# Kernel tuning notes

Measured on AMD Instinct MI355X. Metric: run time of the kernel, lower is better.

The kernel has to match this reference:

```python
import jax, jax.numpy as jnp
import numpy as np

N, E, D, H = 50000, 500000, 160, 5
C = D // H          # per-head channels = 32
MLP_H = 50          # hidden_dim of output MLP
NEG_SLOPE = 0.2
EPS = 1e-5


def layer_norm(x, g, b):
    mu = jnp.mean(x, axis=-1, keepdims=True)
    var = jnp.mean((x - mu) ** 2, axis=-1, keepdims=True)
    return (x - mu) / jnp.sqrt(var + EPS) * g + b


def setup_inputs() -> dict:
    key = jax.random.key(0)
    ks = jax.random.split(key, 24)
    s_d = 1.0 / np.sqrt(D)
    s_h = 1.0 / np.sqrt(MLP_H)
    inp = {
        "x": jax.random.normal(ks[0], (N, D), jnp.float32),
        "edge_index": jax.random.randint(ks[1], (2, E), 0, N, jnp.int32),
        "edge_attr": jax.random.normal(ks[2], (E, D), jnp.float32),
        "u": jax.random.normal(ks[3], (1, 16), jnp.float32),
        "batch": jnp.zeros((N,), jnp.int32),
        # GATv2Conv params (lin_l, lin_r, lin_edge, att, out bias)
        "Wl": jax.random.normal(ks[4], (D, H * C), jnp.float32) * s_d,
        "bl": jnp.zeros((H * C,), jnp.float32),
        "Wr": jax.random.normal(ks[5], (D, H * C), jnp.float32) * s_d,
        "br": jnp.zeros((H * C,), jnp.float32),
        "We": jax.random.normal(ks[6], (D, H * C), jnp.float32) * s_d,
        "att": jax.random.normal(ks[7], (H, C), jnp.float32) * (1.0 / np.sqrt(C)),
        "bias": jnp.zeros((H * C,), jnp.float32),
        # norm1
        "g1": jnp.ones((D,), jnp.float32),
        "beta1": jnp.zeros((D,), jnp.float32),
        # output MLP: Linear(D,50) -> SELU -> LN(50) -> Linear(50,D)
        "W1": jax.random.normal(ks[8], (D, MLP_H), jnp.float32) * s_d,
        "b1": jnp.zeros((MLP_H,), jnp.float32),
        "gm": jnp.ones((MLP_H,), jnp.float32),
        "bm": jnp.zeros((MLP_H,), jnp.float32),
        "W2": jax.random.normal(ks[9], (MLP_H, D), jnp.float32) * s_h,
        "b2": jnp.zeros((D,), jnp.float32),
        # norm2
        "g2": jnp.ones((D,), jnp.float32),
        "beta2": jnp.zeros((D,), jnp.float32),
    }
    return inp


def gatv2(x, edge_index, edge_attr, Wl, bl, Wr, br, We, att, bias):
    src, dst = edge_index[0], edge_index[1]
    xl = (x @ Wl + bl).reshape(N, H, C)   # source transform (x_j)
    xr = (x @ Wr + br).reshape(N, H, C)   # target transform (x_i)
    ea = (edge_attr @ We).reshape(E, H, C)
    m = xl[src] + xr[dst] + ea            # [E,H,C]
    score = jnp.einsum('ehc,hc->eh', jax.nn.leaky_relu(m, NEG_SLOPE), att)  # [E,H]
    # softmax over incoming edges of each destination node
    smax = jax.ops.segment_max(score, dst, num_segments=N)  # [N,H]
    sexp = jnp.exp(score - smax[dst])
    ssum = jax.ops.segment_sum(sexp, dst, num_segments=N)   # [N,H]
    alpha = sexp / jnp.where(ssum == 0.0, 1.0, ssum)[dst]   # [E,H]
    out = jax.ops.segment_sum(xl[src] * alpha[:, :, None], dst, num_segments=N)
    return out.reshape(N, H * C) + bias


def reference(x, edge_index, edge_attr, u, batch,
              Wl, bl, Wr, br, We, att, bias,
              g1, beta1, W1, b1, gm, bm, W2, b2, g2, beta2):
    attn = gatv2(x, edge_index, edge_attr, Wl, bl, Wr, br, We, att, bias)
    h = layer_norm(x + attn, g1, beta1)
    mlp = layer_norm(jax.nn.selu(h @ W1 + b1), gm, bm) @ W2 + b2
    return layer_norm(h + mlp, g2, beta2)
```

## Files before the change

kernel.cpp:

```cpp
#include <hip/hip_runtime.h>

#define NNODES 50000
#define NEDGES 500000
#define DIM    160
#define NHEAD  5
#define MLPH   50

typedef __bf16 bf16x8 __attribute__((ext_vector_type(8)));
typedef float  f32x4  __attribute__((ext_vector_type(4)));

#define PB_WLT   0
#define PB_WRT   25600
#define PB_WET   51200
#define PB_W1    76800
#define PB_W2    84800
#define PB_VEC   92800
#define PB_SMALL 94240
#define PB_TOTAL 94400

struct Ptrs {
    const void *Wl, *Wr, *We;
    const void *bl, *br, *att, *bias, *g1, *beta1;
    const void *W1, *b1, *gm, *bm, *W2, *b2, *g2, *beta2;
};

__device__ __forceinline__ float ldany(const void* p, long i, bool f32) {
    return f32 ? ((const float*)p)[i] : (float)(((const __bf16*)p)[i]);
}

__global__ void detect_kernel(const unsigned short* __restrict__ xs, int* __restrict__ flag) {
    __shared__ int red[4];
    int cnt = 0;
    for (int i = threadIdx.x; i < 65536; i += 256) {
        unsigned e = (xs[i] >> 7) & 0xFFu;
        if (e >= 137u) cnt++;
    }
    for (int off = 1; off < 64; off <<= 1) cnt += __shfl_xor(cnt, off, 64);
    if ((threadIdx.x & 63) == 0) red[threadIdx.x >> 6] = cnt;
    __syncthreads();
    if (threadIdx.x == 0) flag[0] = (red[0] + red[1] + red[2] + red[3] > 1000) ? 1 : 0;
}

__global__ void prep_kernel(Ptrs p, __bf16* __restrict__ pb, const int* __restrict__ flag) {
    const bool f32 = flag[0] != 0;
    int i = blockIdx.x * 256 + threadIdx.x;
    if (i < 76800) {
        int which = i / 25600, r = i - which * 25600;
        int n = r / DIM, k = r - n * DIM;
        const void* w = which == 0 ? p.Wl : which == 1 ? p.Wr : p.We;
        pb[i] = (__bf16)ldany(w, (long)k * DIM + n, f32);
    } else if (i < 84800) {
        pb[i] = (__bf16)ldany(p.W1, i - PB_W1, f32);
    } else if (i < 92800) {
        pb[i] = (__bf16)ldany(p.W2, i - PB_W2, f32);
    } else if (i < 94240) {
        int t = i - PB_VEC, which = t / DIM, off = t - which * DIM;
        const void* v = which == 0 ? p.bl : which == 1 ? p.br : which == 2 ? p.att :
                        which == 3 ? p.bias : which == 4 ? p.g1 : which == 5 ? p.beta1 :
                        which == 6 ? p.b2 : which == 7 ? p.g2 : p.beta2;
        pb[i] = (__bf16)ldany(v, off, f32);
    } else if (i < 94390) {
        int t = i - PB_SMALL;
        const void* v = t < 50 ? p.b1 : t < 100 ? p.gm : p.bm;
        pb[i] = (__bf16)ldany(v, t % 50, f32);
    }
}

template <bool DO_SCORE>
__global__ __launch_bounds__(256, 2) void gemm160(
    const void* __restrict__ A, long M,
    const __bf16* __restrict__ Bt,
    const __bf16* __restrict__ bias,
    __bf16* __restrict__ Cout,
    const __bf16* __restrict__ xl, const __bf16* __restrict__ xr,
    const int* __restrict__ src, const int* __restrict__ dst,
    const __bf16* __restrict__ att, float* __restrict__ score,
    int* __restrict__ cursor, int* __restrict__ psrc,
    const int* __restrict__ flag)
{
    __shared__ __bf16 Bts[DIM * DIM];
    __shared__ __bf16 As[128 * 32];
    const bool aF32 = flag[0] != 0;
    const int tid  = threadIdx.x;
    const int wave = tid >> 6, lane = tid & 63;
    const int quad = lane >> 4, l16 = lane & 15;
    const long blockRow = (long)blockIdx.x * 128;

    {
        const uint4* g = (const uint4*)Bt;
        uint4* s = (uint4*)Bts;
        for (int i = tid; i < DIM * DIM / 8; i += 256) s[i] = g[i];
    }

    const f32x4 zero4 = {0.f, 0.f, 0.f, 0.f};
    f32x4 acc[2][10];
#pragma unroll
    for (int r = 0; r < 2; r++)
#pragma unroll
        for (int n = 0; n < 10; n++) acc[r][n] = zero4;

    for (int k0 = 0; k0 < DIM; k0 += 32) {
        __syncthreads();
        for (int c = tid; c < 512; c += 256) {
            int row = c >> 2, col = (c & 3) * 8;
            long gr = blockRow + row;
            if (!aF32) {
                uint4 v = {0u, 0u, 0u, 0u};
                if (gr < M) v = *(const uint4*)((const __bf16*)A + gr * DIM + k0 + col);
                ((uint4*)As)[c] = v;
            } else {
                bf16x8 t = {};
                if (gr < M) {
                    const float* ap = (const float*)A + gr * DIM + k0 + col;
                    float4 f0 = *(const float4*)ap;
                    float4 f1 = *(const float4*)(ap + 4);
                    t[0] = (__bf16)f0.x; t[1] = (__bf16)f0.y;
                    t[2] = (__bf16)f0.z; t[3] = (__bf16)f0.w;
                    t[4] = (__bf16)f1.x; t[5] = (__bf16)f1.y;
                    t[6] = (__bf16)f1.z; t[7] = (__bf16)f1.w;
                }
                *(bf16x8*)(((uint4*)As) + c) = t;
            }
        }
        __syncthreads();
        bf16x8 a0 = *(const bf16x8*)(As + (wave * 32 + l16) * 32 + quad * 8);
        bf16x8 a1 = *(const bf16x8*)(As + (wave * 32 + 16 + l16) * 32 + quad * 8);
#pragma unroll
        for (int n = 0; n < 10; n++) {
            bf16x8 b = *(const bf16x8*)(Bts + (n * 16 + l16) * DIM + k0 + quad * 8);
            acc[0][n] = __builtin_amdgcn_mfma_f32_16x16x32_bf16(a0, b, acc[0][n], 0, 0, 0);
            acc[1][n] = __builtin_amdgcn_mfma_f32_16x16x32_bf16(a1, b, acc[1][n], 0, 0, 0);
        }
    }

    if (!DO_SCORE) {
#pragma unroll
        for (int r = 0; r < 2; r++)
#pragma unroll
            for (int n = 0; n < 10; n++) {
                int col = n * 16 + l16;
                float bv = (float)bias[col];
#pragma unroll
                for (int reg = 0; reg < 4; reg++) {
                    long row = blockRow + wave * 32 + r * 16 + quad * 4 + reg;
                    if (row < M) Cout[row * DIM + col] = (__bf16)(acc[r][n][reg] + bv);
                }
            }
    } else {
#pragma unroll
        for (int r = 0; r < 2; r++) {
            long erow[4]; int sv[4], dv[4]; int slot[4] = {0, 0, 0, 0};
#pragma unroll
            for (int reg = 0; reg < 4; reg++) {
                erow[reg] = blockRow + wave * 32 + r * 16 + quad * 4 + reg;
                long e = erow[reg] < M ? erow[reg] : M - 1;
                sv[reg] = src[e]; dv[reg] = dst[e];
            }
            if (l16 == 0) {
#pragma unroll
                for (int reg = 0; reg < 4; reg++)
                    if (erow[reg] < M) slot[reg] = atomicAdd(&cursor[dv[reg]], 1);
            }
#pragma unroll
            for (int hh = 0; hh < NHEAD; hh++) {
                float sacc[4] = {0.f, 0.f, 0.f, 0.f};
#pragma unroll
                for (int sub = 0; sub < 2; sub++) {
                    int n = hh * 2 + sub;
                    int col = n * 16 + l16;
                    float av = (float)att[col];
#pragma unroll
                    for (int reg = 0; reg < 4; reg++) {
                        float m = acc[r][n][reg]
                                + (float)xl[(long)sv[reg] * DIM + col]
                                + (float)xr[(long)dv[reg] * DIM + col];
                        m = m > 0.f ? m : 0.2f * m;
                        sacc[reg] += m * av;
                    }
                }
#pragma unroll
                for (int off = 1; off < 16; off <<= 1)
#pragma unroll
                    for (int reg = 0; reg < 4; reg++)
                        sacc[reg] += __shfl_xor(sacc[reg], off, 64);
                if (l16 == 0) {
#pragma unroll
                    for (int reg = 0; reg < 4; reg++)
                        if (erow[reg] < M) score[(long)slot[reg] * NHEAD + hh] = sacc[reg];
                }
            }
            if (l16 == 0) {
#pragma unroll
                for (int reg = 0; reg < 4; reg++)
                    if (erow[reg] < M) psrc[slot[reg]] = sv[reg];
            }
        }
    }
}

__global__ void hist_kernel(const int* __restrict__ dst, int* __restrict__ deg) {
    int e = blockIdx.x * 256 + threadIdx.x;
    if (e < NEDGES) atomicAdd(&deg[dst[e]], 1);
}

__global__ __launch_bounds__(256) void scan_kernel(const int* __restrict__ deg,
                                                   int* __restrict__ offs,
                                                   int* __restrict__ cursor) {
    __shared__ int part[256];
    const int t = threadIdx.x;
    const int chunk = (NNODES + 255) / 256;
    int beg = t * chunk;
    int end = beg + chunk; if (end > NNODES) end = NNODES;
    int s = 0;
    for (int i = beg; i < end; i++) s += deg[i];
    part[t] = s;
    __syncthreads();
    for (int off = 1; off < 256; off <<= 1) {
        int v = 0;
        if (t >= off) v = part[t - off];
        __syncthreads();
        part[t] += v;
        __syncthreads();
    }
    int run = (t == 0) ? 0 : part[t - 1];
    for (int i = beg; i < end; i++) {
        offs[i] = run; cursor[i] = run;
        run += deg[i];
    }
    if (t == 255) offs[NNODES] = run;
}

__global__ __launch_bounds__(256) void node_kernel(
    const int* __restrict__ offs, const int* __restrict__ psrc,
    const float* __restrict__ score,
    const __bf16* __restrict__ xl, const void* __restrict__ x,
    const __bf16* __restrict__ pb, const int* __restrict__ flag,
    __bf16* __restrict__ hout)
{
    const bool f32 = flag[0] != 0;
    const __bf16* bias  = pb + PB_VEC + 3 * DIM;
    const __bf16* g1    = pb + PB_VEC + 4 * DIM;
    const __bf16* beta1 = pb + PB_VEC + 5 * DIM;
    const int lane = threadIdx.x & 63;
    const long n = (long)blockIdx.x * 4 + (threadIdx.x >> 6);
    const int beg = offs[n], end = offs[n + 1];
    const int deg = end - beg;

    float mx[NHEAD];
#pragma unroll
    for (int h = 0; h < NHEAD; h++) mx[h] = -1e30f;
    for (int j = lane; j < deg; j += 64) {
        const float* sp = score + (long)(beg + j) * NHEAD;
#pragma unroll
        for (int h = 0; h < NHEAD; h++) mx[h] = fmaxf(mx[h], sp[h]);
    }
#pragma unroll
    for (int h = 0; h < NHEAD; h++)
#pragma unroll
        for (int off = 1; off < 64; off <<= 1)
            mx[h] = fmaxf(mx[h], __shfl_xor(mx[h], off, 64));

    float sm[NHEAD] = {0.f, 0.f, 0.f, 0.f, 0.f};
    float accv[3] = {0.f, 0.f, 0.f};
    for (int j0 = 0; j0 < deg; j0 += 64) {
        const int cn = min(deg - j0, 64);
        float w[NHEAD]; int si = 0;
        if (lane < cn) {
            const float* sp = score + (long)(beg + j0 + lane) * NHEAD;
#pragma unroll
            for (int h = 0; h < NHEAD; h++) {
                w[h] = expf(sp[h] - mx[h]);
                sm[h] += w[h];
            }
            si = psrc[beg + j0 + lane];
        } else {
#pragma unroll
            for (int h = 0; h < NHEAD; h++) w[h] = 0.f;
        }
        for (int j = 0; j < cn; j++) {
            const int sj = __shfl(si, j, 64);
            const float w0 = __shfl(w[0], j, 64);
            const float w1 = __shfl(w[1], j, 64);
            const float w2 = __shfl(w[2], j, 64);
            const float w3 = __shfl(w[3], j, 64);
            const float w4 = __shfl(w[4], j, 64);
            const __bf16* xrow = xl + (long)sj * DIM;
            accv[0] += (lane < 32 ? w0 : w1) * (float)xrow[lane];
            accv[1] += (lane < 32 ? w2 : w3) * (float)xrow[lane + 64];
            if (lane < 32) accv[2] += w4 * (float)xrow[lane + 128];
        }
    }
#pragma unroll
    for (int h = 0; h < NHEAD; h++)
#pragma unroll
        for (int off = 1; off < 64; off <<= 1)
            sm[h] += __shfl_xor(sm[h], off, 64);
    float ism[NHEAD];
#pragma unroll
    for (int h = 0; h < NHEAD; h++) ism[h] = sm[h] > 0.f ? 1.f / sm[h] : 0.f;
    accv[0] *= lane < 32 ? ism[0] : ism[1];
    accv[1] *= lane < 32 ? ism[2] : ism[3];
    accv[2] *= ism[4];

    const int nch = (lane < 32) ? 3 : 2;
    float v[3]; float s1 = 0.f, s2 = 0.f;
    for (int c = 0; c < nch; c++) {
        int ch = lane + c * 64;
        float xv = f32 ? ((const float*)x)[n * DIM + ch]
                       : (float)(((const __bf16*)x)[n * DIM + ch]);
        float t = accv[c] + (float)bias[ch] + xv;
        v[c] = t; s1 += t; s2 += t * t;
    }
    for (int off = 1; off < 64; off <<= 1) {
        s1 += __shfl_xor(s1, off, 64);
        s2 += __shfl_xor(s2, off, 64);
    }
    float mu = s1 * (1.f / DIM);
    float var = fmaxf(s2 * (1.f / DIM) - mu * mu, 0.f);
    float rs = rsqrtf(var + 1e-5f);
    for (int c = 0; c < nch; c++) {
        int ch = lane + c * 64;
        hout[n * DIM + ch] = (__bf16)((v[c] - mu) * rs * (float)g1[ch] + (float)beta1[ch]);
    }
}

__global__ __launch_bounds__(256, 2) void mlp_kernel(
    const __bf16* __restrict__ hmat, const __bf16* __restrict__ pb,
    float* __restrict__ out)
{
    __shared__ __bf16 W1s[DIM * MLPH];
    __shared__ __bf16 W2s[MLPH * DIM];
    __shared__ float hrow[4][DIM];
    __shared__ float zrow[4][MLPH];
    const __bf16* W1 = pb + PB_W1;
    const __bf16* W2 = pb + PB_W2;
    const __bf16* b2 = pb + PB_VEC + 6 * DIM;
    const __bf16* g2 = pb + PB_VEC + 7 * DIM;
    const __bf16* beta2 = pb + PB_VEC + 8 * DIM;
    const __bf16* b1 = pb + PB_SMALL;
    const __bf16* gm = pb + PB_SMALL + 50;
    const __bf16* bm = pb + PB_SMALL + 100;
    const int tid = threadIdx.x, wave = tid >> 6, lane = tid & 63;
    for (int i = tid; i < DIM * MLPH / 8; i += 256) {
        ((uint4*)W1s)[i] = ((const uint4*)W1)[i];
        ((uint4*)W2s)[i] = ((const uint4*)W2)[i];
    }
    __syncthreads();
    const int nch = (lane < 32) ? 3 : 2;
    for (int it = 0; it < 4; it++) {
        long n = (long)blockIdx.x * 16 + it * 4 + wave;
        float hv[3];
        for (int c = 0; c < nch; c++) {
            int ch = lane + c * 64;
            float t = (float)hmat[n * DIM + ch];
            hv[c] = t; hrow[wave][ch] = t;
        }
        __syncthreads();
        float z = 0.f;
        if (lane < MLPH) {
            z = (float)b1[lane];
            for (int k = 0; k < DIM; k++) z += hrow[wave][k] * (float)W1s[k * MLPH + lane];
            const float SC = 1.0507009873554805f, AL = 1.6732632423543772f;
            z = (z > 0.f) ? SC * z : SC * AL * (expf(z) - 1.f);
        }
        float s1 = (lane < MLPH) ? z : 0.f, s2 = (lane < MLPH) ? z * z : 0.f;
        for (int off = 1; off < 64; off <<= 1) {
            s1 += __shfl_xor(s1, off, 64);
            s2 += __shfl_xor(s2, off, 64);
        }
        float mu = s1 * (1.f / MLPH);
        float var = fmaxf(s2 * (1.f / MLPH) - mu * mu, 0.f);
        float rs = rsqrtf(var + 1e-5f);
        if (lane < MLPH) zrow[wave][lane] = (z - mu) * rs * (float)gm[lane] + (float)bm[lane];
        __syncthreads();
        float y[3], t1 = 0.f, t2 = 0.f;
        for (int c = 0; c < nch; c++) {
            int ch = lane + c * 64;
            float o = (float)b2[ch];
            for (int j = 0; j < MLPH; j++) o += zrow[wave][j] * (float)W2s[j * DIM + ch];
            float yy = hv[c] + o;
            y[c] = yy; t1 += yy; t2 += yy * yy;
        }
        for (int off = 1; off < 64; off <<= 1) {
            t1 += __shfl_xor(t1, off, 64);
            t2 += __shfl_xor(t2, off, 64);
        }
        float mu2 = t1 * (1.f / DIM);
        float var2 = fmaxf(t2 * (1.f / DIM) - mu2 * mu2, 0.f);
        float rs2 = rsqrtf(var2 + 1e-5f);
        for (int c = 0; c < nch; c++) {
            int ch = lane + c * 64;
            out[n * DIM + ch] = (y[c] - mu2) * rs2 * (float)g2[ch] + (float)beta2[ch];
        }
        __syncthreads();
    }
}

extern "C" void kernel_launch(void* const* d_in, const int* in_sizes, int n_in,
                              void* d_out, int out_size, void* d_ws, size_t ws_size,
                              hipStream_t stream)
{
    const void* x   = d_in[0];
    const int*  ei  = (const int*)d_in[1];
    const void* ea  = d_in[2];
    Ptrs p;
    p.Wl = d_in[5];  p.bl = d_in[6];  p.Wr = d_in[7];  p.br = d_in[8];
    p.We = d_in[9];  p.att = d_in[10]; p.bias = d_in[11];
    p.g1 = d_in[12]; p.beta1 = d_in[13];
    p.W1 = d_in[14]; p.b1 = d_in[15]; p.gm = d_in[16]; p.bm = d_in[17];
    p.W2 = d_in[18]; p.b2 = d_in[19]; p.g2 = d_in[20]; p.beta2 = d_in[21];
    const int* srcp = ei;
    const int* dstp = ei + NEDGES;

    char* ws = (char*)d_ws;
    int*    flag   = (int*)ws;    ws += 16;
    __bf16* pb     = (__bf16*)ws; ws += (size_t)PB_TOTAL * 2;
    int*    deg    = (int*)ws;    ws += (size_t)NNODES * 4;
    int*    offs   = (int*)ws;    ws += (size_t)(NNODES + 1) * 4 + 12;
    int*    cursor = (int*)ws;    ws += (size_t)NNODES * 4;
    int*    psrc   = (int*)ws;    ws += (size_t)NEDGES * 4;
    float*  score  = (float*)ws;  ws += (size_t)NEDGES * NHEAD * 4;
    __bf16* xl     = (__bf16*)ws; ws += (size_t)NNODES * DIM * 2;
    __bf16* xr     = (__bf16*)ws; ws += (size_t)NNODES * DIM * 2;
    __bf16* hbuf   = xr;
    const size_t NEEDED = (size_t)(ws - (char*)d_ws);

    if (ws_size < NEEDED) {
        return;
    }

    (void)hipMemsetAsync(deg, 0, (size_t)NNODES * 4, stream);

    detect_kernel<<<1, 256, 0, stream>>>((const unsigned short*)x, flag);
    prep_kernel<<<369, 256, 0, stream>>>(p, pb, flag);

    const int gemmN = (NNODES + 127) / 128;
    const int gemmE = (NEDGES + 127) / 128;
    gemm160<false><<<gemmN, 256, 0, stream>>>(x, NNODES, pb + PB_WLT, pb + PB_VEC + 0 * DIM, xl,
                                              nullptr, nullptr, nullptr, nullptr, nullptr, nullptr,
                                              nullptr, nullptr, flag);
    gemm160<false><<<gemmN, 256, 0, stream>>>(x, NNODES, pb + PB_WRT, pb + PB_VEC + 1 * DIM, xr,
                                              nullptr, nullptr, nullptr, nullptr, nullptr, nullptr,
                                              nullptr, nullptr, flag);

    hist_kernel<<<(NEDGES + 255) / 256, 256, 0, stream>>>(dstp, deg);
    scan_kernel<<<1, 256, 0, stream>>>(deg, offs, cursor);

    gemm160<true><<<gemmE, 256, 0, stream>>>(ea, NEDGES, pb + PB_WET, nullptr, nullptr,
                                             xl, xr, srcp, dstp, pb + PB_VEC + 2 * DIM, score,
                                             cursor, psrc, flag);

    node_kernel<<<NNODES / 4, 256, 0, stream>>>(offs, psrc, score, xl, x, pb, flag, hbuf);

    mlp_kernel<<<NNODES / 16, 256, 0, stream>>>(hbuf, pb, (float*)d_out);
}
```

Before: 1.086 ms.

## Load GEMM A operands directly into registers with prefetch, pad B smem, widen scan

The gemm160 kernel no longer stages A tiles through shared memory. Each lane loads its own A fragments straight from global memory into registers: the fp32 path double-buffers the next K chunk, and the bf16 path preloads all K chunks before the B copy. This removes per-K-step __syncthreads. The B tile is stored with a padded row stride of 168 to avoid LDS bank conflicts, and launch bounds are raised to 3 blocks per CU. The single-block scan is also widened from 256 to 1024 threads to shorten each thread's serial chunk. The trade-off is higher register pressure from the held fragments, which may spill under the new occupancy target.

```diff
diff --git a/kernel.cpp b/kernel.cpp
--- a/kernel.cpp
+++ b/kernel.cpp
@@ -67,7 +67,7 @@
 }
 
 template <bool DO_SCORE>
-__global__ __launch_bounds__(256, 2) void gemm160(
+__global__ __launch_bounds__(256, 3) void gemm160(
     const void* __restrict__ A, long M,
     const __bf16* __restrict__ Bt,
     const __bf16* __restrict__ bias,
@@ -78,19 +78,18 @@
     int* __restrict__ cursor, int* __restrict__ psrc,
     const int* __restrict__ flag)
 {
-    __shared__ __bf16 Bts[DIM * DIM];
-    __shared__ __bf16 As[128 * 32];
+    constexpr int BROW = 168;
+    __shared__ __bf16 Bts[DIM * BROW];
     const bool aF32 = flag[0] != 0;
     const int tid  = threadIdx.x;
     const int wave = tid >> 6, lane = tid & 63;
     const int quad = lane >> 4, l16 = lane & 15;
     const long blockRow = (long)blockIdx.x * 128;
 
-    {
-        const uint4* g = (const uint4*)Bt;
-        uint4* s = (uint4*)Bts;
-        for (int i = tid; i < DIM * DIM / 8; i += 256) s[i] = g[i];
-    }
+    long row0 = blockRow + wave * 32 + l16;
+    long row1 = row0 + 16;
+    const long cr0 = row0 < M ? row0 : M - 1;
+    const long cr1 = row1 < M ? row1 : M - 1;
 
     const f32x4 zero4 = {0.f, 0.f, 0.f, 0.f};
     f32x4 acc[2][10];
@@ -99,37 +98,71 @@
 #pragma unroll
         for (int n = 0; n < 10; n++) acc[r][n] = zero4;
 
-    for (int k0 = 0; k0 < DIM; k0 += 32) {
-        __syncthreads();
-        for (int c = tid; c < 512; c += 256) {
-            int row = c >> 2, col = (c & 3) * 8;
-            long gr = blockRow + row;
-            if (!aF32) {
-                uint4 v = {0u, 0u, 0u, 0u};
-                if (gr < M) v = *(const uint4*)((const __bf16*)A + gr * DIM + k0 + col);
-                ((uint4*)As)[c] = v;
-            } else {
-                bf16x8 t = {};
-                if (gr < M) {
-                    const float* ap = (const float*)A + gr * DIM + k0 + col;
-                    float4 f0 = *(const float4*)ap;
-                    float4 f1 = *(const float4*)(ap + 4);
-                    t[0] = (__bf16)f0.x; t[1] = (__bf16)f0.y;
-                    t[2] = (__bf16)f0.z; t[3] = (__bf16)f0.w;
-                    t[4] = (__bf16)f1.x; t[5] = (__bf16)f1.y;
-                    t[6] = (__bf16)f1.z; t[7] = (__bf16)f1.w;
-                }
-                *(bf16x8*)(((uint4*)As) + c) = t;
-            }
-        }
-        __syncthreads();
-        bf16x8 a0 = *(const bf16x8*)(As + (wave * 32 + l16) * 32 + quad * 8);
-        bf16x8 a1 = *(const bf16x8*)(As + (wave * 32 + 16 + l16) * 32 + quad * 8);
-#pragma unroll
-        for (int n = 0; n < 10; n++) {
-            bf16x8 b = *(const bf16x8*)(Bts + (n * 16 + l16) * DIM + k0 + quad * 8);
-            acc[0][n] = __builtin_amdgcn_mfma_f32_16x16x32_bf16(a0, b, acc[0][n], 0, 0, 0);
-            acc[1][n] = __builtin_amdgcn_mfma_f32_16x16x32_bf16(a1, b, acc[1][n], 0, 0, 0);
+    if (aF32) {
+        const float* A0 = (const float*)A + cr0 * DIM + quad * 8;
+        const float* A1 = (const float*)A + cr1 * DIM + quad * 8;
+        float4 buf[2][2][2];
+        buf[0][0][0] = *(const float4*)(A0);
+        buf[0][0][1] = *(const float4*)(A0 + 4);
+        buf[0][1][0] = *(const float4*)(A1);
+        buf[0][1][1] = *(const float4*)(A1 + 4);
+        for (int i = tid; i < DIM * DIM / 8; i += 256) {
+            int row = i / 20, c = i - row * 20;
+            *(uint4*)(Bts + row * BROW + c * 8) = ((const uint4*)Bt)[i];
+        }
+        __syncthreads();
+#pragma unroll
+        for (int kk = 0; kk < 5; kk++) {
+            const int k0 = kk * 32;
+            if (kk < 4) {
+                buf[(kk + 1) & 1][0][0] = *(const float4*)(A0 + k0 + 32);
+                buf[(kk + 1) & 1][0][1] = *(const float4*)(A0 + k0 + 36);
+                buf[(kk + 1) & 1][1][0] = *(const float4*)(A1 + k0 + 32);
+                buf[(kk + 1) & 1][1][1] = *(const float4*)(A1 + k0 + 36);
+            }
+            bf16x8 a0, a1;
+            {
+                float4 f0 = buf[kk & 1][0][0], f1 = buf[kk & 1][0][1];
+                a0[0] = (__bf16)f0.x; a0[1] = (__bf16)f0.y;
+                a0[2] = (__bf16)f0.z; a0[3] = (__bf16)f0.w;
+                a0[4] = (__bf16)f1.x; a0[5] = (__bf16)f1.y;
+                a0[6] = (__bf16)f1.z; a0[7] = (__bf16)f1.w;
+                f0 = buf[kk & 1][1][0]; f1 = buf[kk & 1][1][1];
+                a1[0] = (__bf16)f0.x; a1[1] = (__bf16)f0.y;
+                a1[2] = (__bf16)f0.z; a1[3] = (__bf16)f0.w;
+                a1[4] = (__bf16)f1.x; a1[5] = (__bf16)f1.y;
+                a1[6] = (__bf16)f1.z; a1[7] = (__bf16)f1.w;
+            }
+#pragma unroll
+            for (int n = 0; n < 10; n++) {
+                bf16x8 b = *(const bf16x8*)(Bts + (n * 16 + l16) * BROW + k0 + quad * 8);
+                acc[0][n] = __builtin_amdgcn_mfma_f32_16x16x32_bf16(a0, b, acc[0][n], 0, 0, 0);
+                acc[1][n] = __builtin_amdgcn_mfma_f32_16x16x32_bf16(a1, b, acc[1][n], 0, 0, 0);
+            }
+        }
+    } else {
+        const __bf16* A0 = (const __bf16*)A + cr0 * DIM + quad * 8;
+        const __bf16* A1 = (const __bf16*)A + cr1 * DIM + quad * 8;
+        bf16x8 af[5][2];
+#pragma unroll
+        for (int kk = 0; kk < 5; kk++) {
+            af[kk][0] = *(const bf16x8*)(A0 + kk * 32);
+            af[kk][1] = *(const bf16x8*)(A1 + kk * 32);
+        }
+        for (int i = tid; i < DIM * DIM / 8; i += 256) {
+            int row = i / 20, c = i - row * 20;
+            *(uint4*)(Bts + row * BROW + c * 8) = ((const uint4*)Bt)[i];
+        }
+        __syncthreads();
+#pragma unroll
+        for (int kk = 0; kk < 5; kk++) {
+            const int k0 = kk * 32;
+#pragma unroll
+            for (int n = 0; n < 10; n++) {
+                bf16x8 b = *(const bf16x8*)(Bts + (n * 16 + l16) * BROW + k0 + quad * 8);
+                acc[0][n] = __builtin_amdgcn_mfma_f32_16x16x32_bf16(af[kk][0], b, acc[0][n], 0, 0, 0);
+                acc[1][n] = __builtin_amdgcn_mfma_f32_16x16x32_bf16(af[kk][1], b, acc[1][n], 0, 0, 0);
+            }
         }
     }
 
@@ -203,19 +236,21 @@
     if (e < NEDGES) atomicAdd(&deg[dst[e]], 1);
 }
 
-__global__ __launch_bounds__(256) void scan_kernel(const int* __restrict__ deg,
-                                                   int* __restrict__ offs,
-                                                   int* __restrict__ cursor) {
-    __shared__ int part[256];
+__global__ __launch_bounds__(1024) void scan_kernel(const int* __restrict__ deg,
+                                                    int* __restrict__ offs,
+                                                    int* __restrict__ cursor) {
+    __shared__ int part[1024];
     const int t = threadIdx.x;
-    const int chunk = (NNODES + 255) / 256;
+    const int chunk = (NNODES + 1023) / 1024;
     int beg = t * chunk;
-    int end = beg + chunk; if (end > NNODES) end = NNODES;
+    int end = beg + chunk;
+    if (beg > NNODES) beg = NNODES;
+    if (end > NNODES) end = NNODES;
     int s = 0;
     for (int i = beg; i < end; i++) s += deg[i];
     part[t] = s;
     __syncthreads();
-    for (int off = 1; off < 256; off <<= 1) {
+    for (int off = 1; off < 1024; off <<= 1) {
         int v = 0;
         if (t >= off) v = part[t - off];
         __syncthreads();
@@ -227,7 +262,7 @@
         offs[i] = run; cursor[i] = run;
         run += deg[i];
     }
-    if (t == 255) offs[NNODES] = run;
+    if (t == 1023) offs[NNODES] = run;
 }
 
 __global__ __launch_bounds__(256) void node_kernel(
@@ -444,7 +479,7 @@
                                               nullptr, nullptr, flag);
 
     hist_kernel<<<(NEDGES + 255) / 256, 256, 0, stream>>>(dstp, deg);
-    scan_kernel<<<1, 256, 0, stream>>>(deg, offs, cursor);
+    scan_kernel<<<1, 1024, 0, stream>>>(deg, offs, cursor);
 
     gemm160<true><<<gemmE, 256, 0, stream>>>(ea, NEDGES, pb + PB_WET, nullptr, nullptr,
                                              xl, xr, srcp, dstp, pb + PB_VEC + 2 * DIM, score,
```

Result: faster. 1.056 ms (-2.7%).
